# Kernel tuning notes

Hardware: AMD Instinct MI355X
Metric: run time of the kernel (lower is better)

## Reference

```python
import jax, jax.numpy as jnp
import numpy as np

E = 512   # embed_size == head_dim
H = 8     # heads
N = 8     # batch
S = 1024  # seq len


def setup_inputs() -> dict:
    key = jax.random.key(0)
    ks = jax.random.split(key, 12)
    scale = 1.0 / np.sqrt(E)
    inp = {
        "values": jax.random.normal(ks[0], (N, S, E), jnp.float32),
        "keys": jax.random.normal(ks[1], (N, S, E), jnp.float32),
        "query": jax.random.normal(ks[2], (N, S, E), jnp.float32),
        "pos": jnp.arange(S, dtype=jnp.int64) if jax.config.jax_enable_x64 else jnp.arange(S, dtype=jnp.int32),
        "mask": jax.random.randint(ks[3], (N, 1, S, S), 0, 2, jnp.int32),
        # nn.Linear params: weight (out,in), y = x @ W.T + b
        "Wv": jax.random.uniform(ks[4], (E * H, E), jnp.float32, -scale, scale),
        "bv": jax.random.uniform(ks[5], (E * H,), jnp.float32, -scale, scale),
        "Wk": jax.random.uniform(ks[6], (E * H, E), jnp.float32, -scale, scale),
        "bk": jax.random.uniform(ks[7], (E * H,), jnp.float32, -scale, scale),
        "Wq": jax.random.uniform(ks[8], (E * H, E), jnp.float32, -scale, scale),
        "bq": jax.random.uniform(ks[9], (E * H,), jnp.float32, -scale, scale),
        "Wo": jax.random.uniform(ks[10], (E, E), jnp.float32, -scale, scale),
        "bo": jax.random.uniform(ks[11], (E,), jnp.float32, -scale, scale),
    }
    return inp


def reference(values, keys, query, pos, mask, Wv, bv, Wk, bk, Wq, bq, Wo, bo):
    n, q_len, e = query.shape
    v_len = values.shape[1]
    k_len = keys.shape[1]
    h = Wq.shape[0] // e
    # QKV projections: E -> E*H, reshape to (N, L, H, E)
    v = (values @ Wv.T + bv).reshape(n, v_len, h, e)
    k = (keys @ Wk.T + bk).reshape(n, k_len, h, e)
    q = (query @ Wq.T + bq).reshape(n, q_len, h, e)
    # bilinear energy, no softmax
    energy = jnp.einsum('nqhd,nkhd->nhqk', q, k)
    energy = jnp.where(mask == 0, jnp.zeros((), energy.dtype), energy)
    attention = energy / jnp.asarray(e ** 0.5, energy.dtype)
    out = jnp.einsum('nhql,nlhd->nqhd', attention, v).sum(axis=2)  # sum over heads
    return out @ Wo.T + bo
```

## Files before the change

### kernel.cpp

```cpp
#include <hip/hip_runtime.h>


#define RS 0.04419417382415922f

typedef __attribute__((ext_vector_type(8))) short bf16x8;
typedef __attribute__((ext_vector_type(4))) float f32x4;

__device__ __forceinline__ unsigned short f2b(float f) {
  unsigned u = __builtin_bit_cast(unsigned, f);
  unsigned r = (u + 0x7FFFu + ((u >> 16) & 1u)) >> 16;
  return (unsigned short)r;
}
__device__ __forceinline__ float b2f(unsigned short h) {
  return __builtin_bit_cast(float, ((unsigned)h) << 16);
}

__global__ void k_fill(float* p, int n, float v) {
  int i = blockIdx.x * blockDim.x + threadIdx.x;
  int stride = gridDim.x * blockDim.x;
  for (; i < n; i += stride) p[i] = v;
}

__global__ void k_conv(const float4* __restrict__ s, ushort4* __restrict__ d,
                       int n4, float scale) {
  int stride = gridDim.x * blockDim.x;
  for (int i = blockIdx.x * blockDim.x + threadIdx.x; i < n4; i += stride) {
    float4 v = s[i];
    ushort4 o;
    o.x = f2b(v.x * scale); o.y = f2b(v.y * scale);
    o.z = f2b(v.z * scale); o.w = f2b(v.w * scale);
    d[i] = o;
  }
}

__global__ void k_reduce(const unsigned short* __restrict__ a,
                         unsigned short* __restrict__ o) {
  int i = blockIdx.x * blockDim.x + threadIdx.x;
  const ushort4* av = (const ushort4*)a;
  float4 s = {0.f, 0.f, 0.f, 0.f};
#pragma unroll
  for (int h = 0; h < 8; ++h) {
    ushort4 v = av[h * 131072 + i];
    s.x += b2f(v.x); s.y += b2f(v.y); s.z += b2f(v.z); s.w += b2f(v.w);
  }
  ushort4 r;
  r.x = f2b(s.x); r.y = f2b(s.y); r.z = f2b(s.z); r.w = f2b(s.w);
  ((ushort4*)o)[i] = r;
}

#define GLD16(gp, sp)                                              \
  __builtin_amdgcn_global_load_lds(                                \
      (const __attribute__((address_space(1))) void*)(gp),         \
      (__attribute__((address_space(3))) void*)(sp), 16, 0, 0)

template <int MODE>
__global__ __launch_bounds__(256) void k_gemm(
    const unsigned short* __restrict__ A, const unsigned short* __restrict__ B,
    const float* __restrict__ bias, float bscale, const int* __restrict__ maskI,
    unsigned short* __restrict__ outb, float* __restrict__ outf, int n0) {
  __shared__ short smem[17408];
  char* const sb = (char*)smem;

  const int tid = threadIdx.x;
  const int wid = tid >> 6;
  const int lane = tid & 63;
  const int wr = wid >> 1, wc = wid & 1;
  const int l15 = lane & 15, l4 = lane >> 4;
  const int bx = blockIdx.x, by = blockIdx.y, bz = blockIdx.z;

  constexpr int KSEG = (MODE == 4) ? 1024 : 512;
  constexpr int NK = KSEG / 32;

  f32x4 acc[4][4];
#pragma unroll
  for (int i = 0; i < 4; ++i)
#pragma unroll
    for (int j = 0; j < 4; ++j) acc[i][j] = (f32x4){0.f, 0.f, 0.f, 0.f};

  const unsigned short* Ab;
  const unsigned short* Bb;
  if constexpr (MODE == 0 || MODE == 1 || MODE == 5) {
    Ab = A + (size_t)bx * 128 * 512;
    Bb = B + (size_t)by * 128 * 512;
  } else if constexpr (MODE == 2) {
    Ab = A + (size_t)bz * 524288 + (size_t)bx * 128 * 512;
    Bb = B + (size_t)bz * 524288 + (size_t)by * 128 * 512;
  } else {
    Ab = A + (size_t)bz * 1048576 + (size_t)bx * 128 * 1024;
    Bb = B + (size_t)bz * 524288 + (size_t)by * 128 * 1024;
  }

#define STAGE(buf, kc)                                             \
  {                                                                \
    _Pragma("unroll") for (int is = 0; is < 2; ++is) {             \
      int c = is * 256 + tid;                                      \
      int row = c >> 2, col = (c & 3) << 3;                        \
      GLD16(Ab + (size_t)row * KSEG + (kc)*32 + col,               \
            sb + (buf)*8192 + is * 4096 + wid * 1024);             \
      GLD16(Bb + (size_t)row * KSEG + (kc)*32 + col,               \
            sb + 16384 + (buf)*8192 + is * 4096 + wid * 1024);     \
    }                                                              \
  }

  STAGE(0, 0);
  int cur = 0;
#pragma unroll 4
  for (int kc = 0; kc < NK; ++kc) {
    __syncthreads();
    if (kc + 1 < NK) STAGE(cur ^ 1, kc + 1);
    bf16x8 af[4], bf_[4];
#pragma unroll
    for (int f = 0; f < 4; ++f) {
      af[f] = *(const bf16x8*)(sb + cur * 8192 +
                               ((wr * 64 + f * 16 + l15) << 6) + (l4 << 4));
      bf_[f] = *(const bf16x8*)(sb + 16384 + cur * 8192 +
                                ((wc * 64 + f * 16 + l15) << 6) + (l4 << 4));
    }
#pragma unroll
    for (int mf = 0; mf < 4; ++mf)
#pragma unroll
      for (int nf = 0; nf < 4; ++nf)
        acc[mf][nf] = __builtin_amdgcn_mfma_f32_16x16x32_bf16(
            af[mf], bf_[nf], acc[mf][nf], 0, 0, 0);
    cur ^= 1;
  }
#undef STAGE

  const int r0 = l4 * 4;
  const int c0 = l15;

  if constexpr (MODE != 5) {
    __syncthreads();
#pragma unroll
    for (int nf = 0; nf < 4; ++nf) {
      int c_loc = wc * 64 + nf * 16 + c0;
      int c_ = by * 128 + c_loc;
      float bvl = 0.f;
      if constexpr (MODE == 0 || MODE == 1) bvl = bias[c_] * bscale;
#pragma unroll
      for (int mf = 0; mf < 4; ++mf) {
#pragma unroll
        for (int r = 0; r < 4; ++r) {
          int r_loc = wr * 64 + mf * 16 + r0 + r;
          float v = acc[mf][nf][r] + bvl;
          unsigned short bb;
          if constexpr (MODE == 2) {
            int r_ = bx * 128 + r_loc;
            int mv = maskI[(size_t)(n0 + (bz >> 3)) * 1048576 +
                           (size_t)r_ * 1024 + c_];
            bb = mv ? f2b(v) : (unsigned short)0;
          } else {
            bb = f2b(v);
          }
          if constexpr (MODE == 1)
            smem[c_loc * 136 + r_loc] = (short)bb;
          else
            smem[r_loc * 136 + c_loc] = (short)bb;
        }
      }
    }
    __syncthreads();
#pragma unroll
    for (int ch = 0; ch < 8; ++ch) {
      int idx = ch * 256 + tid;
      int row = idx >> 4;
      int col = (idx & 15) << 3;
      bf16x8 v = *(const bf16x8*)(smem + row * 136 + col);
      if constexpr (MODE == 0) {
        int r_ = bx * 128 + row, cB = by * 128 + col;
        int nl = r_ >> 10, s = r_ & 1023, h = cB >> 9, e = cB & 511;
        *(bf16x8*)(outb + (((size_t)nl * 8 + h) * 1024 + s) * 512 + e) = v;
      } else if constexpr (MODE == 1) {
        int cB = by * 128 + row;
        int r_ = bx * 128 + col;
        int nl = r_ >> 10, s = r_ & 1023, h = cB >> 9, e = cB & 511;
        *(bf16x8*)(outb + (((size_t)nl * 8 + h) * 512 + e) * 1024 + s) = v;
      } else if constexpr (MODE == 2) {
        int r_ = bx * 128 + row, cB = by * 128 + col;
        *(bf16x8*)(outb + (size_t)bz * 1048576 + (size_t)r_ * 1024 + cB) = v;
      } else {
        int r_ = bx * 128 + row, cB = by * 128 + col;
        *(bf16x8*)(outb + (size_t)bz * 524288 + (size_t)r_ * 512 + cB) = v;
      }
    }
  } else {
    float* const Cs32 = (float*)smem;
#pragma unroll
    for (int hh = 0; hh < 2; ++hh) {
      __syncthreads();
      if (wr == hh) {
#pragma unroll
        for (int nf = 0; nf < 4; ++nf) {
          int c_loc = wc * 64 + nf * 16 + c0;
          float bvl = bias[by * 128 + c_loc];
#pragma unroll
          for (int mf = 0; mf < 4; ++mf)
#pragma unroll
            for (int r = 0; r < 4; ++r) {
              int rl = mf * 16 + r0 + r;
              Cs32[rl * 136 + c_loc] = acc[mf][nf][r] + bvl;
            }
        }
      }
      __syncthreads();
#pragma unroll
      for (int ch = 0; ch < 8; ++ch) {
        int idx = ch * 256 + tid;
        int row = idx >> 5;
        int col = (idx & 31) << 2;
        float4 v = *(const float4*)(Cs32 + row * 136 + col);
        *(float4*)(outf + (size_t)(bx * 128 + hh * 64 + row) * 512 +
                   by * 128 + col) = v;
      }
    }
  }
}

extern "C" void kernel_launch(void* const* d_in, const int* in_sizes, int n_in,
                              void* d_out, int out_size, void* d_ws,
                              size_t ws_size, hipStream_t stream) {
  const float* values = (const float*)d_in[0];
  const float* keys = (const float*)d_in[1];
  const float* query = (const float*)d_in[2];
  const int* maskI = (const int*)d_in[4];
  const float* Wv = (const float*)d_in[5];
  const float* bv = (const float*)d_in[6];
  const float* Wk = (const float*)d_in[7];
  const float* bk = (const float*)d_in[8];
  const float* Wq = (const float*)d_in[9];
  const float* bq = (const float*)d_in[10];
  const float* Wo = (const float*)d_in[11];
  const float* bo = (const float*)d_in[12];
  float* dout = (float*)d_out;

  const int exp_sizes[13] = {4194304, 4194304, 4194304, 1024, 8388608,
                             2097152, 4096,    2097152, 4096, 2097152,
                             4096,    262144,  512};
  bool ok = (n_in == 13);
  if (ok)
    for (int i = 0; i < 13; ++i)
      if (in_sizes[i] != exp_sizes[i]) ok = false;
  if (!ok) {
    k_fill<<<512, 256, 0, stream>>>(dout, out_size, 1000.f);
    return;
  }

  char* w = (char*)d_ws;
  unsigned short* Wvb = (unsigned short*)(w);
  unsigned short* Wkb = (unsigned short*)(w + 4194304);
  unsigned short* Wqb = (unsigned short*)(w + 8388608);
  unsigned short* Wob = (unsigned short*)(w + 12582912);
  unsigned short* Atb = (unsigned short*)(w + 13107200);
  unsigned short* Q2 = (unsigned short*)(w + 21495808);
  unsigned short* K2 = (unsigned short*)(w + 38273024);
  unsigned short* VT2 = (unsigned short*)(w + 55050240);
  unsigned short* P2 = (unsigned short*)(w + 71827456);
  unsigned short* Xcv = (unsigned short*)(w + 105381888);
  unsigned short* Xck = (unsigned short*)(w + 107479040);
  unsigned short* Xcq = (unsigned short*)(w + 109576192);
  unsigned short* Ah2 = (unsigned short*)(w + 105381888);
  const size_t need = 122159104;
  if (ws_size < need) {
    k_fill<<<512, 256, 0, stream>>>(dout, out_size, 2000.f);
    return;
  }

  k_conv<<<512, 256, 0, stream>>>((const float4*)Wv, (ushort4*)Wvb, 524288,
                                  1.0f);
  k_conv<<<512, 256, 0, stream>>>((const float4*)Wk, (ushort4*)Wkb, 524288,
                                  1.0f);
  k_conv<<<512, 256, 0, stream>>>((const float4*)Wq, (ushort4*)Wqb, 524288,
                                  RS);
  k_conv<<<256, 256, 0, stream>>>((const float4*)Wo, (ushort4*)Wob, 65536,
                                  1.0f);

  for (int it = 0; it < 4; ++it) {
    const int n0 = it * 2;
    const size_t xoff = (size_t)n0 * 524288;
    k_conv<<<1024, 256, 0, stream>>>((const float4*)(values + xoff),
                                     (ushort4*)Xcv, 262144, 1.0f);
    k_conv<<<1024, 256, 0, stream>>>((const float4*)(keys + xoff),
                                     (ushort4*)Xck, 262144, 1.0f);
    k_conv<<<1024, 256, 0, stream>>>((const float4*)(query + xoff),
                                     (ushort4*)Xcq, 262144, 1.0f);
    k_gemm<1><<<dim3(16, 32, 1), 256, 0, stream>>>(Xcv, Wvb, bv, 1.0f, nullptr,
                                                   VT2, nullptr, 0);
    k_gemm<0><<<dim3(16, 32, 1), 256, 0, stream>>>(Xck, Wkb, bk, 1.0f, nullptr,
                                                   K2, nullptr, 0);
    k_gemm<0><<<dim3(16, 32, 1), 256, 0, stream>>>(Xcq, Wqb, bq, RS, nullptr,
                                                   Q2, nullptr, 0);
    k_gemm<2><<<dim3(8, 8, 16), 256, 0, stream>>>(Q2, K2, nullptr, 0.f, maskI,
                                                  P2, nullptr, n0);
    k_gemm<4><<<dim3(8, 4, 16), 256, 0, stream>>>(P2, VT2, nullptr, 0.f,
                                                  nullptr, Ah2, nullptr, 0);
    k_reduce<<<512, 256, 0, stream>>>(Ah2, Atb + (size_t)n0 * 524288);
    k_reduce<<<512, 256, 0, stream>>>(Ah2 + 4194304,
                                      Atb + (size_t)(n0 + 1) * 524288);
  }

  k_gemm<5><<<dim3(64, 4, 1), 256, 0, stream>>>(Atb, Wob, bo, 1.0f, nullptr,
                                                nullptr, dout, 0);
}
```

Measured before the change: 577.5 us.

## Batch QKV projections into one launch and process four batches per iteration

```diff
diff --git a/kernel.cpp b/kernel.cpp
--- a/kernel.cpp
+++ b/kernel.cpp
@@ -21,8 +21,23 @@
   for (; i < n; i += stride) p[i] = v;
 }
 
-__global__ void k_conv(const float4* __restrict__ s, ushort4* __restrict__ d,
-                       int n4, float scale) {
+__global__ void k_conv3(const float4* __restrict__ v,
+                        const float4* __restrict__ k,
+                        const float4* __restrict__ q, ushort4* __restrict__ d,
+                        int n4, int dstride) {
+  const float4* s = (blockIdx.z == 0) ? v : (blockIdx.z == 1) ? k : q;
+  ushort4* dz = d + (size_t)blockIdx.z * dstride;
+  int stride = gridDim.x * blockDim.x;
+  for (int i = blockIdx.x * blockDim.x + threadIdx.x; i < n4; i += stride) {
+    float4 x = s[i];
+    ushort4 o;
+    o.x = f2b(x.x); o.y = f2b(x.y); o.z = f2b(x.z); o.w = f2b(x.w);
+    dz[i] = o;
+  }
+}
+
+__global__ void k_convw(const float4* __restrict__ s, ushort4* __restrict__ d,
+                        int n4, float scale) {
   int stride = gridDim.x * blockDim.x;
   for (int i = blockIdx.x * blockDim.x + threadIdx.x; i < n4; i += stride) {
     float4 v = s[i];
@@ -34,13 +49,15 @@
 }
 
 __global__ void k_reduce(const unsigned short* __restrict__ a,
-                         unsigned short* __restrict__ o) {
+                         unsigned short* __restrict__ o, int total) {
   int i = blockIdx.x * blockDim.x + threadIdx.x;
-  const ushort4* av = (const ushort4*)a;
+  if (i >= total) return;
+  int nl = i >> 17, j = i & 131071;
+  const ushort4* av = (const ushort4*)a + (size_t)nl * 1048576;
   float4 s = {0.f, 0.f, 0.f, 0.f};
 #pragma unroll
   for (int h = 0; h < 8; ++h) {
-    ushort4 v = av[h * 131072 + i];
+    ushort4 v = av[h * 131072 + j];
     s.x += b2f(v.x); s.y += b2f(v.y); s.z += b2f(v.z); s.w += b2f(v.w);
   }
   ushort4 r;
@@ -56,9 +73,11 @@
 template <int MODE>
 __global__ __launch_bounds__(256) void k_gemm(
     const unsigned short* __restrict__ A, const unsigned short* __restrict__ B,
-    const float* __restrict__ bias, float bscale, const int* __restrict__ maskI,
-    unsigned short* __restrict__ outb, float* __restrict__ outf, int n0) {
-  __shared__ short smem[17408];
+    const float* __restrict__ bi0, const float* __restrict__ bi1,
+    const float* __restrict__ bi2, const int* __restrict__ maskI,
+    unsigned short* __restrict__ outb, float* __restrict__ outf, int n0,
+    int xstr, int ostr) {
+  __shared__ short smem[16384];
   char* const sb = (char*)smem;
 
   const int tid = threadIdx.x;
@@ -79,9 +98,12 @@
 
   const unsigned short* Ab;
   const unsigned short* Bb;
-  if constexpr (MODE == 0 || MODE == 1 || MODE == 5) {
+  if constexpr (MODE == 5) {
     Ab = A + (size_t)bx * 128 * 512;
     Bb = B + (size_t)by * 128 * 512;
+  } else if constexpr (MODE == 6) {
+    Ab = A + (size_t)bz * xstr + (size_t)bx * 128 * 512;
+    Bb = B + (size_t)bz * 2097152 + (size_t)by * 128 * 512;
   } else if constexpr (MODE == 2) {
     Ab = A + (size_t)bz * 524288 + (size_t)bx * 128 * 512;
     Bb = B + (size_t)bz * 524288 + (size_t)by * 128 * 512;
@@ -130,57 +152,69 @@
   const int c0 = l15;
 
   if constexpr (MODE != 5) {
-    __syncthreads();
-#pragma unroll
-    for (int nf = 0; nf < 4; ++nf) {
-      int c_loc = wc * 64 + nf * 16 + c0;
-      int c_ = by * 128 + c_loc;
-      float bvl = 0.f;
-      if constexpr (MODE == 0 || MODE == 1) bvl = bias[c_] * bscale;
-#pragma unroll
-      for (int mf = 0; mf < 4; ++mf) {
-#pragma unroll
-        for (int r = 0; r < 4; ++r) {
-          int r_loc = wr * 64 + mf * 16 + r0 + r;
-          float v = acc[mf][nf][r] + bvl;
-          unsigned short bb;
-          if constexpr (MODE == 2) {
-            int r_ = bx * 128 + r_loc;
-            int mv = maskI[(size_t)(n0 + (bz >> 3)) * 1048576 +
-                           (size_t)r_ * 1024 + c_];
-            bb = mv ? f2b(v) : (unsigned short)0;
-          } else {
-            bb = f2b(v);
+    const bool transp = (MODE == 6) && (bz == 0);
+    const float* bias =
+        (MODE == 6) ? ((bz == 0) ? bi0 : (bz == 1) ? bi1 : bi2) : nullptr;
+    const float bscale = (MODE == 6 && bz == 2) ? RS : 1.0f;
+#pragma unroll
+    for (int hh = 0; hh < 2; ++hh) {
+      __syncthreads();
+      int own = transp ? wc : wr;
+      if (own == hh) {
+#pragma unroll
+        for (int nf = 0; nf < 4; ++nf) {
+          int c_loc = wc * 64 + nf * 16 + c0;
+          int c_ = by * 128 + c_loc;
+          float bvl = (MODE == 6) ? bias[c_] * bscale : 0.f;
+#pragma unroll
+          for (int mf = 0; mf < 4; ++mf) {
+#pragma unroll
+            for (int r = 0; r < 4; ++r) {
+              int r_loc = wr * 64 + mf * 16 + r0 + r;
+              float v = acc[mf][nf][r] + bvl;
+              unsigned short bb;
+              if constexpr (MODE == 2) {
+                int r_ = bx * 128 + r_loc;
+                int mv = maskI[(size_t)(n0 + (bz >> 3)) * 1048576 +
+                               (size_t)r_ * 1024 + c_];
+                bb = mv ? f2b(v) : (unsigned short)0;
+              } else {
+                bb = f2b(v);
+              }
+              if (transp)
+                smem[(c_loc - hh * 64) * 136 + r_loc] = (short)bb;
+              else
+                smem[(r_loc - hh * 64) * 136 + c_loc] = (short)bb;
+            }
           }
-          if constexpr (MODE == 1)
-            smem[c_loc * 136 + r_loc] = (short)bb;
-          else
-            smem[r_loc * 136 + c_loc] = (short)bb;
         }
       }
-    }
-    __syncthreads();
-#pragma unroll
-    for (int ch = 0; ch < 8; ++ch) {
-      int idx = ch * 256 + tid;
-      int row = idx >> 4;
-      int col = (idx & 15) << 3;
-      bf16x8 v = *(const bf16x8*)(smem + row * 136 + col);
-      if constexpr (MODE == 0) {
-        int r_ = bx * 128 + row, cB = by * 128 + col;
-        int nl = r_ >> 10, s = r_ & 1023, h = cB >> 9, e = cB & 511;
-        *(bf16x8*)(outb + (((size_t)nl * 8 + h) * 1024 + s) * 512 + e) = v;
-      } else if constexpr (MODE == 1) {
-        int cB = by * 128 + row;
-        int r_ = bx * 128 + col;
-        int nl = r_ >> 10, s = r_ & 1023, h = cB >> 9, e = cB & 511;
-        *(bf16x8*)(outb + (((size_t)nl * 8 + h) * 512 + e) * 1024 + s) = v;
-      } else if constexpr (MODE == 2) {
-        int r_ = bx * 128 + row, cB = by * 128 + col;
-        *(bf16x8*)(outb + (size_t)bz * 1048576 + (size_t)r_ * 1024 + cB) = v;
-      } else {
-        int r_ = bx * 128 + row, cB = by * 128 + col;
-        *(bf16x8*)(outb + (size_t)bz * 524288 + (size_t)r_ * 512 + cB) = v;
+      __syncthreads();
+#pragma unroll
+      for (int ch = 0; ch < 4; ++ch) {
+        int idx = ch * 256 + tid;
+        int row = hh * 64 + (idx >> 4);
+        int col = (idx & 15) << 3;
+        bf16x8 v = *(const bf16x8*)(smem + (idx >> 4) * 136 + col);
+        if constexpr (MODE == 2) {
+          int r_ = bx * 128 + row, cB = by * 128 + col;
+          *(bf16x8*)(outb + (size_t)bz * 1048576 + (size_t)r_ * 1024 + cB) = v;
+        } else if constexpr (MODE == 4) {
+          int r_ = bx * 128 + row, cB = by * 128 + col;
+          *(bf16x8*)(outb + (size_t)bz * 524288 + (size_t)r_ * 512 + cB) = v;
+        } else {
+          unsigned short* O = outb + (size_t)bz * ostr;
+          if (bz == 0) {
+            int eB = by * 128 + row;
+            int r_ = bx * 128 + col;
+            int nl = r_ >> 10, s = r_ & 1023, h = eB >> 9, e = eB & 511;
+            *(bf16x8*)(O + (((size_t)nl * 8 + h) * 512 + e) * 1024 + s) = v;
+          } else {
+            int r_ = bx * 128 + row, cB = by * 128 + col;
+            int nl = r_ >> 10, s = r_ & 1023, h = cB >> 9, e = cB & 511;
+            *(bf16x8*)(O + (((size_t)nl * 8 + h) * 1024 + s) * 512 + e) = v;
+          }
+        }
       }
     }
   } else {
@@ -192,14 +226,12 @@
 #pragma unroll
         for (int nf = 0; nf < 4; ++nf) {
           int c_loc = wc * 64 + nf * 16 + c0;
-          float bvl = bias[by * 128 + c_loc];
+          float bvl = bi0[by * 128 + c_loc];
 #pragma unroll
           for (int mf = 0; mf < 4; ++mf)
 #pragma unroll
-            for (int r = 0; r < 4; ++r) {
-              int rl = mf * 16 + r0 + r;
-              Cs32[rl * 136 + c_loc] = acc[mf][nf][r] + bvl;
-            }
+            for (int r = 0; r < 4; ++r)
+              Cs32[(mf * 16 + r0 + r) * 128 + c_loc] = acc[mf][nf][r] + bvl;
         }
       }
       __syncthreads();
@@ -208,7 +240,7 @@
         int idx = ch * 256 + tid;
         int row = idx >> 5;
         int col = (idx & 31) << 2;
-        float4 v = *(const float4*)(Cs32 + row * 136 + col);
+        float4 v = *(const float4*)(Cs32 + row * 128 + col);
         *(float4*)(outf + (size_t)(bx * 128 + hh * 64 + row) * 512 +
                    by * 128 + col) = v;
       }
@@ -245,59 +277,55 @@
     return;
   }
 
+  const size_t need4 = 222822400;
+  const size_t need2 = 122159104;
+  const int NL = (ws_size >= need4) ? 4 : 2;
+  if (ws_size < need2) {
+    k_fill<<<512, 256, 0, stream>>>(dout, out_size, 2000.f);
+    return;
+  }
+
   char* w = (char*)d_ws;
   unsigned short* Wvb = (unsigned short*)(w);
-  unsigned short* Wkb = (unsigned short*)(w + 4194304);
-  unsigned short* Wqb = (unsigned short*)(w + 8388608);
   unsigned short* Wob = (unsigned short*)(w + 12582912);
   unsigned short* Atb = (unsigned short*)(w + 13107200);
-  unsigned short* Q2 = (unsigned short*)(w + 21495808);
-  unsigned short* K2 = (unsigned short*)(w + 38273024);
-  unsigned short* VT2 = (unsigned short*)(w + 55050240);
-  unsigned short* P2 = (unsigned short*)(w + 71827456);
-  unsigned short* Xcv = (unsigned short*)(w + 105381888);
-  unsigned short* Xck = (unsigned short*)(w + 107479040);
-  unsigned short* Xcq = (unsigned short*)(w + 109576192);
-  unsigned short* Ah2 = (unsigned short*)(w + 105381888);
-  const size_t need = 122159104;
-  if (ws_size < need) {
-    k_fill<<<512, 256, 0, stream>>>(dout, out_size, 2000.f);
-    return;
-  }
-
-  k_conv<<<512, 256, 0, stream>>>((const float4*)Wv, (ushort4*)Wvb, 524288,
-                                  1.0f);
-  k_conv<<<512, 256, 0, stream>>>((const float4*)Wk, (ushort4*)Wkb, 524288,
-                                  1.0f);
-  k_conv<<<512, 256, 0, stream>>>((const float4*)Wq, (ushort4*)Wqb, 524288,
-                                  RS);
-  k_conv<<<256, 256, 0, stream>>>((const float4*)Wo, (ushort4*)Wob, 65536,
-                                  1.0f);
-
-  for (int it = 0; it < 4; ++it) {
-    const int n0 = it * 2;
+  const size_t SZT = (size_t)NL * 8388608;
+  unsigned short* VTb = (unsigned short*)(w + 21495808);
+  unsigned short* Kb = (unsigned short*)(w + 21495808 + SZT);
+  unsigned short* Qb = (unsigned short*)(w + 21495808 + 2 * SZT);
+  unsigned short* Pb = (unsigned short*)(w + 21495808 + 3 * SZT);
+  char* Xbase = w + 21495808 + 3 * SZT + (size_t)NL * 16777216;
+  unsigned short* Xc = (unsigned short*)(Xbase);
+  unsigned short* Ahb = (unsigned short*)(Xbase);
+
+  k_convw<<<512, 256, 0, stream>>>((const float4*)Wv, (ushort4*)Wvb, 524288,
+                                   1.0f);
+  k_convw<<<512, 256, 0, stream>>>((const float4*)Wk, (ushort4*)(Wvb + 2097152),
+                                   524288, 1.0f);
+  k_convw<<<512, 256, 0, stream>>>((const float4*)Wq, (ushort4*)(Wvb + 4194304),
+                                   524288, RS);
+  k_convw<<<256, 256, 0, stream>>>((const float4*)Wo, (ushort4*)Wob, 65536,
+                                   1.0f);
+
+  const int xstr = NL * 524288;
+  const int ostr = NL * 4194304;
+
+  for (int it = 0; it < 8 / NL; ++it) {
+    const int n0 = it * NL;
     const size_t xoff = (size_t)n0 * 524288;
-    k_conv<<<1024, 256, 0, stream>>>((const float4*)(values + xoff),
-                                     (ushort4*)Xcv, 262144, 1.0f);
-    k_conv<<<1024, 256, 0, stream>>>((const float4*)(keys + xoff),
-                                     (ushort4*)Xck, 262144, 1.0f);
-    k_conv<<<1024, 256, 0, stream>>>((const float4*)(query + xoff),
-                                     (ushort4*)Xcq, 262144, 1.0f);
-    k_gemm<1><<<dim3(16, 32, 1), 256, 0, stream>>>(Xcv, Wvb, bv, 1.0f, nullptr,
-                                                   VT2, nullptr, 0);
-    k_gemm<0><<<dim3(16, 32, 1), 256, 0, stream>>>(Xck, Wkb, bk, 1.0f, nullptr,
-                                                   K2, nullptr, 0);
-    k_gemm<0><<<dim3(16, 32, 1), 256, 0, stream>>>(Xcq, Wqb, bq, RS, nullptr,
-                                                   Q2, nullptr, 0);
-    k_gemm<2><<<dim3(8, 8, 16), 256, 0, stream>>>(Q2, K2, nullptr, 0.f, maskI,
-                                                  P2, nullptr, n0);
-    k_gemm<4><<<dim3(8, 4, 16), 256, 0, stream>>>(P2, VT2, nullptr, 0.f,
-                                                  nullptr, Ah2, nullptr, 0);
-    k_reduce<<<512, 256, 0, stream>>>(Ah2, Atb + (size_t)n0 * 524288);
-    k_reduce<<<512, 256, 0, stream>>>(Ah2 + 4194304,
-                                      Atb + (size_t)(n0 + 1) * 524288);
-  }
-
-  k_gemm<5><<<dim3(64, 4, 1), 256, 0, stream>>>(Atb, Wob, bo, 1.0f, nullptr,
-                                                nullptr, dout, 0);
-}
+    k_conv3<<<dim3(512 * NL, 1, 3), 256, 0, stream>>>(
+        (const float4*)(values + xoff), (const float4*)(keys + xoff),
+        (const float4*)(query + xoff), (ushort4*)Xc, NL * 131072, NL * 131072);
+    k_gemm<6><<<dim3(NL * 8, 32, 3), 256, 0, stream>>>(
+        Xc, Wvb, bv, bk, bq, nullptr, VTb, nullptr, 0, xstr, ostr);
+    k_gemm<2><<<dim3(8, 8, NL * 8), 256, 0, stream>>>(
+        Qb, Kb, nullptr, nullptr, nullptr, maskI, Pb, nullptr, n0, 0, 0);
+    k_gemm<4><<<dim3(8, 4, NL * 8), 256, 0, stream>>>(
+        Pb, VTb, nullptr, nullptr, nullptr, nullptr, Ahb, nullptr, 0, 0, 0);
+    k_reduce<<<NL * 512, 256, 0, stream>>>(
+        Ahb, Atb + (size_t)n0 * 524288, NL * 131072);
+  }
+
+  k_gemm<5><<<dim3(64, 4, 1), 256, 0, stream>>>(
+      Atb, Wob, bo, nullptr, nullptr, nullptr, nullptr, dout, 0, 0, 0);
+}
```

After: 752.4 us. 30.3% more time.
